# Optimization experiments

Hardware: AMD Instinct MI355X
Metric: run time of the kernel (lower is better)

Reference implementation:

```python
import jax, jax.numpy as jnp
import numpy as np

BOARD_H, BOARD_W = 10, 9
NUM_NODES = BOARD_H * BOARD_W  # 90
NUM_HEADS = 4


def _build_base_adjacency():
    adj = np.zeros((NUM_NODES, NUM_NODES), dtype=np.float32)
    for y in range(BOARD_H):
        for x in range(BOARD_W):
            idx = y * BOARD_W + x
            for dy, dx in [(0, 1), (0, -1), (1, 0), (-1, 0)]:
                ny, nx = y + dy, x + dx
                if 0 <= ny < BOARD_H and 0 <= nx < BOARD_W:
                    adj[idx, ny * BOARD_W + nx] = 1.0
            for nx in range(BOARD_W):
                if nx != x and abs(nx - x) <= 4:
                    nidx = y * BOARD_W + nx
                    adj[idx, nidx] = max(adj[idx, nidx], 1.0 / abs(nx - x))
            for ny in range(BOARD_H):
                if ny != y and abs(ny - y) <= 5:
                    nidx = ny * BOARD_W + x
                    adj[idx, nidx] = max(adj[idx, nidx], 1.0 / abs(ny - y))
            adj[idx, idx] = 1.0
    deg = np.clip(adj.sum(-1, keepdims=True), 1.0, None)
    return adj / deg  # (90, 90)


def _pos_encoding():
    px = (np.arange(BOARD_W, dtype=np.float32) / BOARD_W)
    py = (np.arange(BOARD_H, dtype=np.float32) / BOARD_H)
    gx = np.broadcast_to(px[None, :], (BOARD_H, BOARD_W)).reshape(-1)
    gy = np.broadcast_to(py[:, None], (BOARD_H, BOARD_W)).reshape(-1)
    return np.stack([gx, gy], axis=-1)  # (90, 2)


def _gat_layer(x, adj, W, a_src, a_dst, gamma, beta):
    B, N, _ = x.shape
    h = (x @ W).reshape(B, N, NUM_HEADS, -1)          # (B,N,H,D)
    s_src = jnp.einsum('bnhd,hd->bhn', h, a_src)       # (B,H,N)
    s_dst = jnp.einsum('bnhd,hd->bhn', h, a_dst)
    attn = s_src[..., :, None] + s_dst[..., None, :]   # (B,H,N,N)
    attn = jax.nn.leaky_relu(attn, 0.2)
    attn = jnp.where((adj == 0)[None, None], -jnp.inf, attn)
    attn = jax.nn.softmax(attn, axis=-1)
    attn = jnp.nan_to_num(attn, nan=0.0)
    out = jnp.einsum('bhij,bjhd->bihd', attn, h).reshape(B * N, -1)
    # BatchNorm1d in training mode: biased batch stats over (B*N)
    mean = out.mean(0)
    var = out.var(0)
    out = (out - mean) * jax.lax.rsqrt(var + 1e-5) * gamma + beta
    return jax.nn.relu(out.reshape(B, N, -1))


def setup_inputs() -> dict:
    key = jax.random.key(0)
    ks = jax.random.split(key, 16)
    B, F_in, Hd, Dout = 2048, 16, 64, 128
    hdim = Hd // NUM_HEADS
    p = lambda k, s: (jax.random.normal(k, s, dtype=jnp.float32) * 0.1)
    return {
        'board_planes': jax.random.uniform(ks[0], (B, 14, BOARD_H, BOARD_W), dtype=jnp.float32),
        'in_W': p(ks[1], (F_in, Hd)), 'in_b': p(ks[2], (Hd,)),
        'W0': p(ks[3], (Hd, Hd)), 'asrc0': p(ks[4], (NUM_HEADS, hdim)), 'adst0': p(ks[5], (NUM_HEADS, hdim)),
        'g0': jnp.ones((Hd,), jnp.float32), 'b0': jnp.zeros((Hd,), jnp.float32),
        'W1': p(ks[6], (Hd, Hd)), 'asrc1': p(ks[7], (NUM_HEADS, hdim)), 'adst1': p(ks[8], (NUM_HEADS, hdim)),
        'g1': jnp.ones((Hd,), jnp.float32), 'b1': jnp.zeros((Hd,), jnp.float32),
        'out_W': p(ks[9], (Hd, Dout)), 'out_b': p(ks[10], (Dout,)),
    }


def reference(board_planes, in_W, in_b, W0, asrc0, adst0, g0, b0,
              W1, asrc1, adst1, g1, b1, out_W, out_b):
    B = board_planes.shape[0]
    adj = jnp.asarray(_build_base_adjacency())            # (90,90), same for all batches
    nodes = board_planes.reshape(B, 14, NUM_NODES).transpose(0, 2, 1)  # (B,90,14)
    pos = jnp.broadcast_to(jnp.asarray(_pos_encoding())[None], (B, NUM_NODES, 2))
    x = jnp.concatenate([nodes, pos], axis=-1)            # (B,90,16)
    x = x @ in_W + in_b
    x = _gat_layer(x, adj, W0, asrc0, adst0, g0, b0)
    x = _gat_layer(x, adj, W1, asrc1, adst1, g1, b1)
    return x.mean(axis=1) @ out_W + out_b                 # (B,128)
```

## Files before the change

### kernel.cpp

```cpp
#include <hip/hip_runtime.h>
#include <cstdint>


#define BB   2048
#define NN   90
#define NP   96
#define CC   64
#define NH   4
#define HD   16
#define TPB  512
#define DOUT 128
#define SWP  72
#define SHP  72
#define PPITCH 24
#define NSLOT 19

typedef _Float16 f16;
typedef _Float16 f16x4 __attribute__((ext_vector_type(4)));
typedef _Float16 f16x8 __attribute__((ext_vector_type(8)));
typedef float f32x4 __attribute__((ext_vector_type(4)));
union U16x8 { f16x8 v; f16 e[8]; };
union U16x4 { f16x4 v; f16 e[4]; };

#define UNI_BYTES 19712
#define BIG_BYTES 27648

template <int LAYER>
__global__ __launch_bounds__(TPB, 6) void k_gat(
    const float* __restrict__ bp,
    const float* __restrict__ inW,
    const float* __restrict__ inb,
    const float* __restrict__ prevPre,
    const float* __restrict__ stPrev,
    const float* __restrict__ Wl,
    const float* __restrict__ asrc,
    const float* __restrict__ adst,
    float* __restrict__ outPre,
    float* __restrict__ partial,
    float* __restrict__ partialSq)
{
    __shared__ __align__(16) unsigned char uni[UNI_BYTES];
    __shared__ __align__(16) unsigned char big[BIG_BYTES];
    __shared__ float sAs[NH * HD], sAd[NH * HD];
    __shared__ float sSrc[NH][NN], sDst[NH][NN];
    __shared__ float sST[2 * CC];

    f16*   sWt  = (f16*)uni;
    float* sInW = (float*)(uni + 9216);
    float* sInb = (float*)(uni + 13312);
    float* sXr  = (float*)(uni + 13568);
    f16*   sPh  = (f16*)uni;
    float* sRa  = (float*)uni;
    float* sRb  = (float*)(uni + 8192);
    f16*   sx   = (f16*)big;
    float* shF  = (float*)big;

    const int b = blockIdx.x, t = threadIdx.x;
    const int cq = t & 15, ng = t >> 4;
    const int c4 = cq << 2;
    const int jcnt = (ng < NN - 64) ? 3 : 2;

    for (int i = t; i < CC * CC; i += TPB) {
        int k = i >> 6, c = i & 63;
        sWt[c * SWP + k] = (f16)Wl[i];
    }
    if (t < NH * HD) { sAs[t] = asrc[t]; sAd[t] = adst[t]; }

    if (t < (NP - NN) * (SHP / 4)) {
        int r = t / (SHP / 4), q = t % (SHP / 4);
        f16x4 z = {(f16)0, (f16)0, (f16)0, (f16)0};
        *(f16x4*)&sx[(NN + r) * SHP + q * 4] = z;
    }

    if (LAYER == 0) {
        for (int i = t; i < 16 * CC; i += TPB) sInW[i] = inW[i];
        if (t < CC) sInb[t] = inb[t];
        const float* bpb = bp + (size_t)b * (14 * NN);
        for (int i = t; i < 14 * NN; i += TPB) {
            int p = i / NN, n = i - p * NN;
            sXr[n * 17 + p] = bpb[i];
        }
        if (t < NN) {
            int y = t / 9, x = t - y * 9;
            sXr[t * 17 + 14] = (float)x / 9.0f;
            sXr[t * 17 + 15] = (float)y / 10.0f;
        }
    } else {
        if (t < 2 * CC) sST[t] = stPrev[t];
    }
    __syncthreads();

    if (LAYER == 0) {
        const int n0 = ng, n1 = ng + 32, n2 = (jcnt == 3) ? ng + 64 : ng;
        float acc[3][4] = {};
        #pragma unroll
        for (int k = 0; k < 16; k++) {
            float4 w = *(const float4*)&sInW[k * CC + c4];
            float x0 = sXr[n0 * 17 + k], x1 = sXr[n1 * 17 + k], x2 = sXr[n2 * 17 + k];
            acc[0][0] = fmaf(x0, w.x, acc[0][0]); acc[0][1] = fmaf(x0, w.y, acc[0][1]);
            acc[0][2] = fmaf(x0, w.z, acc[0][2]); acc[0][3] = fmaf(x0, w.w, acc[0][3]);
            acc[1][0] = fmaf(x1, w.x, acc[1][0]); acc[1][1] = fmaf(x1, w.y, acc[1][1]);
            acc[1][2] = fmaf(x1, w.z, acc[1][2]); acc[1][3] = fmaf(x1, w.w, acc[1][3]);
            acc[2][0] = fmaf(x2, w.x, acc[2][0]); acc[2][1] = fmaf(x2, w.y, acc[2][1]);
            acc[2][2] = fmaf(x2, w.z, acc[2][2]); acc[2][3] = fmaf(x2, w.w, acc[2][3]);
        }
        for (int j = 0; j < jcnt; j++) {
            int n = ng + 32 * j;
            f16x4 o;
            o.x = (f16)(acc[j][0] + sInb[c4 + 0]);
            o.y = (f16)(acc[j][1] + sInb[c4 + 1]);
            o.z = (f16)(acc[j][2] + sInb[c4 + 2]);
            o.w = (f16)(acc[j][3] + sInb[c4 + 3]);
            *(f16x4*)&sx[n * SHP + c4] = o;
        }
    } else {
        const float4* pv4 = (const float4*)(prevPre + (size_t)b * (NN * CC));
        for (int i4 = t; i4 < NN * CC / 4; i4 += TPB) {
            float4 v = pv4[i4];
            int n = i4 >> 4, c = (i4 & 15) << 2;
            float a0 = fmaf(v.x, sST[c + 0], sST[CC + c + 0]);
            float a1 = fmaf(v.y, sST[c + 1], sST[CC + c + 1]);
            float a2 = fmaf(v.z, sST[c + 2], sST[CC + c + 2]);
            float a3 = fmaf(v.w, sST[c + 3], sST[CC + c + 3]);
            f16x4 o;
            o.x = (f16)(a0 > 0.0f ? a0 : 0.0f);
            o.y = (f16)(a1 > 0.0f ? a1 : 0.0f);
            o.z = (f16)(a2 > 0.0f ? a2 : 0.0f);
            o.w = (f16)(a3 > 0.0f ? a3 : 0.0f);
            *(f16x4*)&sx[n * SHP + c] = o;
        }
    }
    __syncthreads();

    {
        const int w = t >> 6, lane = t & 63;
        const int lr = lane & 15, lg = lane >> 4;
        const int nt = w & 3, m0 = w >> 2;
        const f16x8 bf0 = *(const f16x8*)&sWt[(nt * 16 + lr) * SWP + lg * 8];
        const f16x8 bf1 = *(const f16x8*)&sWt[(nt * 16 + lr) * SWP + 32 + lg * 8];
        f16x8 af0[3], af1[3];
        #pragma unroll
        for (int mi = 0; mi < 3; mi++) {
            const int mt = m0 + 2 * mi;
            af0[mi] = *(const f16x8*)&sx[(mt * 16 + lr) * SHP + lg * 8];
            af1[mi] = *(const f16x8*)&sx[(mt * 16 + lr) * SHP + 32 + lg * 8];
        }
        __syncthreads();
        #pragma unroll
        for (int mi = 0; mi < 3; mi++) {
            const int mt = m0 + 2 * mi;
            f32x4 acc = {0.0f, 0.0f, 0.0f, 0.0f};
            acc = __builtin_amdgcn_mfma_f32_16x16x32_f16(af0[mi], bf0, acc, 0, 0, 0);
            acc = __builtin_amdgcn_mfma_f32_16x16x32_f16(af1[mi], bf1, acc, 0, 0, 0);
            const int row = mt * 16 + lg * 4, col = nt * 16 + lr;
            shF[(row + 0) * SHP + col] = acc[0];
            shF[(row + 1) * SHP + col] = acc[1];
            shF[(row + 2) * SHP + col] = acc[2];
            shF[(row + 3) * SHP + col] = acc[3];
        }
    }
    __syncthreads();

    if (t < NH * NN) {
        int hh = t / NN, n = t - hh * NN;
        const float4* hv = (const float4*)&shF[n * SHP + hh * HD];
        float a = 0.0f, d = 0.0f;
        #pragma unroll
        for (int m = 0; m < 4; m++) {
            float4 h4 = hv[m];
            a = fmaf(h4.x, sAs[hh * HD + 4 * m + 0], a);
            a = fmaf(h4.y, sAs[hh * HD + 4 * m + 1], a);
            a = fmaf(h4.z, sAs[hh * HD + 4 * m + 2], a);
            a = fmaf(h4.w, sAs[hh * HD + 4 * m + 3], a);
            d = fmaf(h4.x, sAd[hh * HD + 4 * m + 0], d);
            d = fmaf(h4.y, sAd[hh * HD + 4 * m + 1], d);
            d = fmaf(h4.z, sAd[hh * HD + 4 * m + 2], d);
            d = fmaf(h4.w, sAd[hh * HD + 4 * m + 3], d);
        }
        sSrc[hh][n] = a; sDst[hh][n] = d;
    }
    __syncthreads();

    if (t < NH * NN) {
        int hh = t / NN, n = t - hh * NN;
        int y = n / 9, x = n - y * 9;
        float si = sSrc[hh][n];
        float e[NSLOT];
        #pragma unroll
        for (int xx = 0; xx < 9; xx++) {
            int dx = xx > x ? xx - x : x - xx;
            float ee = si + sDst[hh][y * 9 + xx];
            ee = ee > 0.0f ? ee : 0.2f * ee;
            e[xx] = (dx <= 4) ? ee : -1e30f;
        }
        #pragma unroll
        for (int yy = 0; yy < 10; yy++) {
            int dy = yy > y ? yy - y : y - yy;
            float ee = si + sDst[hh][yy * 9 + x];
            ee = ee > 0.0f ? ee : 0.2f * ee;
            e[9 + yy] = (dy >= 1 && dy <= 5) ? ee : -1e30f;
        }
        float m = e[0];
        #pragma unroll
        for (int k = 1; k < NSLOT; k++) m = fmaxf(m, e[k]);
        float s = 0.0f;
        f16* pr = &sPh[(hh * NN + n) * PPITCH];
        #pragma unroll
        for (int k = 0; k < NSLOT; k++) {
            float p = __expf(e[k] - m);
            s += p;
            pr[k] = (f16)p;
        }
        sSrc[hh][n] = 1.0f / s;
    }
    __syncthreads();

    const int hh2 = cq >> 2;
    float lsum[4] = {}, lsq[4] = {};
    float* op = outPre + (size_t)b * (NN * CC);
    for (int j = 0; j < jcnt; j++) {
        int n = ng + 32 * j;
        int y = n / 9, x = n - y * 9;
        float inv = sSrc[hh2][n];
        const f16* pr = &sPh[(hh2 * NN + n) * PPITCH];
        U16x8 pA, pB; U16x4 pT;
        pA.v = *(const f16x8*)pr;
        pB.v = *(const f16x8*)(pr + 8);
        pT.v = *(const f16x4*)(pr + 16);
        float a0 = 0.0f, a1 = 0.0f, a2 = 0.0f, a3 = 0.0f;
        #pragma unroll
        for (int xx = 0; xx < 9; xx++) {
            float p = (xx < 8) ? (float)pA.e[xx] : (float)pB.e[0];
            float4 h4 = *(const float4*)&shF[(y * 9 + xx) * SHP + c4];
            a0 = fmaf(p, h4.x, a0); a1 = fmaf(p, h4.y, a1);
            a2 = fmaf(p, h4.z, a2); a3 = fmaf(p, h4.w, a3);
        }
        #pragma unroll
        for (int yy = 0; yy < 10; yy++) {
            int k = 9 + yy;
            float p = (k < 16) ? (float)pB.e[k - 8] : (float)pT.e[k - 16];
            float4 h4 = *(const float4*)&shF[(yy * 9 + x) * SHP + c4];
            a0 = fmaf(p, h4.x, a0); a1 = fmaf(p, h4.y, a1);
            a2 = fmaf(p, h4.z, a2); a3 = fmaf(p, h4.w, a3);
        }
        a0 *= inv; a1 *= inv; a2 *= inv; a3 *= inv;
        float4 o; o.x = a0; o.y = a1; o.z = a2; o.w = a3;
        *(float4*)&op[n * CC + c4] = o;
        lsum[0] += a0; lsum[1] += a1; lsum[2] += a2; lsum[3] += a3;
        lsq[0] = fmaf(a0, a0, lsq[0]); lsq[1] = fmaf(a1, a1, lsq[1]);
        lsq[2] = fmaf(a2, a2, lsq[2]); lsq[3] = fmaf(a3, a3, lsq[3]);
    }
    __syncthreads();

    #pragma unroll
    for (int q = 0; q < 4; q++) {
        sRa[ng * CC + c4 + q] = lsum[q];
        sRb[ng * CC + c4 + q] = lsq[q];
    }
    __syncthreads();
    if (t < CC) {
        float s = 0.0f, q2 = 0.0f;
        #pragma unroll
        for (int g = 0; g < 32; g++) {
            s  += sRa[g * CC + t];
            q2 += sRb[g * CC + t];
        }
        partial[(size_t)b * CC + t] = s;
        partialSq[(size_t)b * CC + t] = q2;
    }
}

__global__ __launch_bounds__(256) void k_stats(
    const float* __restrict__ partial, const float* __restrict__ partialSq,
    const float* __restrict__ gamma, const float* __restrict__ beta,
    float* __restrict__ st)
{
    const int c = blockIdx.x, t = threadIdx.x;
    float s = 0.0f, q = 0.0f;
    for (int b = t; b < BB; b += 256) {
        s += partial[(size_t)b * CC + c];
        q += partialSq[(size_t)b * CC + c];
    }
    __shared__ float rs[256], rq[256];
    rs[t] = s; rq[t] = q;
    __syncthreads();
    for (int o = 128; o > 0; o >>= 1) {
        if (t < o) { rs[t] += rs[t + o]; rq[t] += rq[t + o]; }
        __syncthreads();
    }
    if (t == 0) {
        const float cntInv = 1.0f / (float)(BB * NN);
        float mean = rs[0] * cntInv;
        float var  = rq[0] * cntInv - mean * mean;
        float sc = gamma[c] * rsqrtf(var + 1e-5f);
        st[c] = sc;
        st[CC + c] = beta[c] - mean * sc;
    }
}

__global__ __launch_bounds__(256) void k_final(
    const float* __restrict__ pre, const float* __restrict__ st,
    const float* __restrict__ outW, const float* __restrict__ outb,
    float* __restrict__ out)
{
    __shared__ float sM[CC];
    __shared__ float sPart[4][CC];
    const int b = blockIdx.x, t = threadIdx.x;
    const int c = t & 63, p = t >> 6;
    const float* pv = pre + (size_t)b * (NN * CC);
    float s = st[c], sft = st[CC + c];
    float a = 0.0f;
    int nBeg = p * 23, nEnd = nBeg + 23 < NN ? nBeg + 23 : NN;
    for (int n = nBeg; n < nEnd; n++) {
        float v = fmaf(pv[n * CC + c], s, sft);
        a += (v > 0.0f ? v : 0.0f);
    }
    sPart[p][c] = a;
    __syncthreads();
    if (t < CC)
        sM[t] = (sPart[0][t] + sPart[1][t] + sPart[2][t] + sPart[3][t]) * (1.0f / (float)NN);
    __syncthreads();
    if (t < DOUT) {
        float acc = outb[t];
        #pragma unroll
        for (int cc2 = 0; cc2 < CC; cc2++) acc = fmaf(sM[cc2], outW[cc2 * DOUT + t], acc);
        out[(size_t)b * DOUT + t] = acc;
    }
}

extern "C" void kernel_launch(void* const* d_in, const int* in_sizes, int n_in,
                              void* d_out, int out_size, void* d_ws, size_t ws_size,
                              hipStream_t stream) {
    (void)in_sizes; (void)n_in; (void)out_size; (void)ws_size;

    const float* bp   = (const float*)d_in[0];
    const float* inW  = (const float*)d_in[1];
    const float* inb  = (const float*)d_in[2];
    const float* W0   = (const float*)d_in[3];
    const float* as0  = (const float*)d_in[4];
    const float* ad0  = (const float*)d_in[5];
    const float* g0   = (const float*)d_in[6];
    const float* b0   = (const float*)d_in[7];
    const float* W1   = (const float*)d_in[8];
    const float* as1  = (const float*)d_in[9];
    const float* ad1  = (const float*)d_in[10];
    const float* g1   = (const float*)d_in[11];
    const float* b1   = (const float*)d_in[12];
    const float* outW = (const float*)d_in[13];
    const float* outb = (const float*)d_in[14];
    float* out = (float*)d_out;

    float* ws = (float*)d_ws;
    float* outPre    = ws;
    float* partial   = outPre + (size_t)BB * NN * CC;
    float* partialSq = partial + (size_t)BB * CC;
    float* st0       = partialSq + (size_t)BB * CC;
    float* st1       = st0 + 2 * CC;

    k_gat<0><<<BB, TPB, 0, stream>>>(bp, inW, inb, nullptr, nullptr,
                                     W0, as0, ad0, outPre, partial, partialSq);
    k_stats<<<CC, 256, 0, stream>>>(partial, partialSq, g0, b0, st0);
    k_gat<1><<<BB, TPB, 0, stream>>>(nullptr, nullptr, nullptr, outPre, st0,
                                     W1, as1, ad1, outPre, partial, partialSq);
    k_stats<<<CC, 256, 0, stream>>>(partial, partialSq, g1, b1, st1);
    k_final<<<BB, 256, 0, stream>>>(outPre, st1, outW, outb, out);
}
```

Before: 109.0 us.

## Shrink LDS footprint to raise occupancy and read weights from global

Merges the shared buffers into one smaller LDS region by narrowing pitches, storing the raw inputs and attention scores in fp16, and no longer staging the weight matrix, input weights, bias and attention vectors in LDS. Those are now read directly from global memory or cache. The launch bound rises from 6 to 8 blocks per CU. Softmax normalisation moves into the probability write, and the stats reduction uses wave shuffles before an 8-way LDS combine. The extra global reads of the weights and the fp16 score precision are the trade-offs, and a dead f16x4 loop is left behind.

```diff
diff --git a/kernel.cpp b/kernel.cpp
--- a/kernel.cpp
+++ b/kernel.cpp
@@ -10,23 +10,21 @@
 #define HD   16
 #define TPB  512
 #define DOUT 128
-#define SWP  72
-#define SHP  72
-#define PPITCH 24
+#define SXP  72
+#define SHP  68
+#define PPITCH 20
 #define NSLOT 19
 
 typedef _Float16 f16;
 typedef _Float16 f16x4 __attribute__((ext_vector_type(4)));
 typedef _Float16 f16x8 __attribute__((ext_vector_type(8)));
 typedef float f32x4 __attribute__((ext_vector_type(4)));
-union U16x8 { f16x8 v; f16 e[8]; };
 union U16x4 { f16x4 v; f16 e[4]; };
 
-#define UNI_BYTES 19712
-#define BIG_BYTES 27648
+#define LDS_BYTES 40832
 
 template <int LAYER>
-__global__ __launch_bounds__(TPB, 6) void k_gat(
+__global__ __launch_bounds__(TPB, 8) void k_gat(
     const float* __restrict__ bp,
     const float* __restrict__ inW,
     const float* __restrict__ inb,
@@ -39,51 +37,40 @@
     float* __restrict__ partial,
     float* __restrict__ partialSq)
 {
-    __shared__ __align__(16) unsigned char uni[UNI_BYTES];
-    __shared__ __align__(16) unsigned char big[BIG_BYTES];
-    __shared__ float sAs[NH * HD], sAd[NH * HD];
-    __shared__ float sSrc[NH][NN], sDst[NH][NN];
-    __shared__ float sST[2 * CC];
-
-    f16*   sWt  = (f16*)uni;
-    float* sInW = (float*)(uni + 9216);
-    float* sInb = (float*)(uni + 13312);
-    float* sXr  = (float*)(uni + 13568);
+    __shared__ __align__(16) unsigned char lds[LDS_BYTES];
+    float* shF  = (float*)lds;
+    f16*   sx   = (f16*)lds;
+    unsigned char* uni = lds + 24480;
+    f16*   sXr  = (f16*)uni;
     f16*   sPh  = (f16*)uni;
     float* sRa  = (float*)uni;
-    float* sRb  = (float*)(uni + 8192);
-    f16*   sx   = (f16*)big;
-    float* shF  = (float*)big;
+    float* sRb  = (float*)(uni + 2048);
+    f16*   sSrcH = (f16*)(lds + 38880);
+    f16*   sDstH = (f16*)(lds + 39600);
+    float* sST   = (float*)(lds + 40320);
 
     const int b = blockIdx.x, t = threadIdx.x;
     const int cq = t & 15, ng = t >> 4;
     const int c4 = cq << 2;
     const int jcnt = (ng < NN - 64) ? 3 : 2;
-
-    for (int i = t; i < CC * CC; i += TPB) {
-        int k = i >> 6, c = i & 63;
-        sWt[c * SWP + k] = (f16)Wl[i];
-    }
-    if (t < NH * HD) { sAs[t] = asrc[t]; sAd[t] = adst[t]; }
-
-    if (t < (NP - NN) * (SHP / 4)) {
-        int r = t / (SHP / 4), q = t % (SHP / 4);
+    const int lane = t & 63, wv = t >> 6;
+    const int lr = lane & 15, lg = lane >> 4;
+
+    if (t < (NP - NN) * (SXP / 4)) {
+        int r = t / (SXP / 4), q = t - r * (SXP / 4);
         f16x4 z = {(f16)0, (f16)0, (f16)0, (f16)0};
-        *(f16x4*)&sx[(NN + r) * SHP + q * 4] = z;
-    }
-
+        *(f16x4*)&sx[(NN + r) * SXP + q * 4] = z;
+    }
     if (LAYER == 0) {
-        for (int i = t; i < 16 * CC; i += TPB) sInW[i] = inW[i];
-        if (t < CC) sInb[t] = inb[t];
         const float* bpb = bp + (size_t)b * (14 * NN);
         for (int i = t; i < 14 * NN; i += TPB) {
             int p = i / NN, n = i - p * NN;
-            sXr[n * 17 + p] = bpb[i];
+            sXr[n * 17 + p] = (f16)bpb[i];
         }
         if (t < NN) {
             int y = t / 9, x = t - y * 9;
-            sXr[t * 17 + 14] = (float)x / 9.0f;
-            sXr[t * 17 + 15] = (float)y / 10.0f;
+            sXr[t * 17 + 14] = (f16)((float)x / 9.0f);
+            sXr[t * 17 + 15] = (f16)((float)y / 10.0f);
         }
     } else {
         if (t < 2 * CC) sST[t] = stPrev[t];
@@ -92,11 +79,14 @@
 
     if (LAYER == 0) {
         const int n0 = ng, n1 = ng + 32, n2 = (jcnt == 3) ? ng + 64 : ng;
+        const float4* inW4 = (const float4*)inW;
         float acc[3][4] = {};
-        #pragma unroll
+        #pragma unroll 4
         for (int k = 0; k < 16; k++) {
-            float4 w = *(const float4*)&sInW[k * CC + c4];
-            float x0 = sXr[n0 * 17 + k], x1 = sXr[n1 * 17 + k], x2 = sXr[n2 * 17 + k];
+            float4 w = inW4[k * 16 + cq];
+            float x0 = (float)sXr[n0 * 17 + k];
+            float x1 = (float)sXr[n1 * 17 + k];
+            float x2 = (float)sXr[n2 * 17 + k];
             acc[0][0] = fmaf(x0, w.x, acc[0][0]); acc[0][1] = fmaf(x0, w.y, acc[0][1]);
             acc[0][2] = fmaf(x0, w.z, acc[0][2]); acc[0][3] = fmaf(x0, w.w, acc[0][3]);
             acc[1][0] = fmaf(x1, w.x, acc[1][0]); acc[1][1] = fmaf(x1, w.y, acc[1][1]);
@@ -104,14 +94,15 @@
             acc[2][0] = fmaf(x2, w.x, acc[2][0]); acc[2][1] = fmaf(x2, w.y, acc[2][1]);
             acc[2][2] = fmaf(x2, w.z, acc[2][2]); acc[2][3] = fmaf(x2, w.w, acc[2][3]);
         }
+        float4 bias = *(const float4*)&inb[c4];
         for (int j = 0; j < jcnt; j++) {
             int n = ng + 32 * j;
             f16x4 o;
-            o.x = (f16)(acc[j][0] + sInb[c4 + 0]);
-            o.y = (f16)(acc[j][1] + sInb[c4 + 1]);
-            o.z = (f16)(acc[j][2] + sInb[c4 + 2]);
-            o.w = (f16)(acc[j][3] + sInb[c4 + 3]);
-            *(f16x4*)&sx[n * SHP + c4] = o;
+            o.x = (f16)(acc[j][0] + bias.x);
+            o.y = (f16)(acc[j][1] + bias.y);
+            o.z = (f16)(acc[j][2] + bias.z);
+            o.w = (f16)(acc[j][3] + bias.w);
+            *(f16x4*)&sx[n * SXP + c4] = o;
         }
     } else {
         const float4* pv4 = (const float4*)(prevPre + (size_t)b * (NN * CC));
@@ -127,23 +118,25 @@
             o.y = (f16)(a1 > 0.0f ? a1 : 0.0f);
             o.z = (f16)(a2 > 0.0f ? a2 : 0.0f);
             o.w = (f16)(a3 > 0.0f ? a3 : 0.0f);
-            *(f16x4*)&sx[n * SHP + c] = o;
+            *(f16x4*)&sx[n * SXP + c] = o;
         }
     }
     __syncthreads();
 
     {
-        const int w = t >> 6, lane = t & 63;
-        const int lr = lane & 15, lg = lane >> 4;
-        const int nt = w & 3, m0 = w >> 2;
-        const f16x8 bf0 = *(const f16x8*)&sWt[(nt * 16 + lr) * SWP + lg * 8];
-        const f16x8 bf1 = *(const f16x8*)&sWt[(nt * 16 + lr) * SWP + 32 + lg * 8];
+        const int nt = wv & 3, m0 = wv >> 2;
+        f16x8 bf0, bf1;
+        #pragma unroll
+        for (int j = 0; j < 8; j++) {
+            bf0[j] = (f16)Wl[(lg * 8 + j) * CC + nt * 16 + lr];
+            bf1[j] = (f16)Wl[(lg * 8 + j + 32) * CC + nt * 16 + lr];
+        }
         f16x8 af0[3], af1[3];
         #pragma unroll
         for (int mi = 0; mi < 3; mi++) {
             const int mt = m0 + 2 * mi;
-            af0[mi] = *(const f16x8*)&sx[(mt * 16 + lr) * SHP + lg * 8];
-            af1[mi] = *(const f16x8*)&sx[(mt * 16 + lr) * SHP + 32 + lg * 8];
+            af0[mi] = *(const f16x8*)&sx[(mt * 16 + lr) * SXP + lg * 8];
+            af1[mi] = *(const f16x8*)&sx[(mt * 16 + lr) * SXP + 32 + lg * 8];
         }
         __syncthreads();
         #pragma unroll
@@ -153,10 +146,9 @@
             acc = __builtin_amdgcn_mfma_f32_16x16x32_f16(af0[mi], bf0, acc, 0, 0, 0);
             acc = __builtin_amdgcn_mfma_f32_16x16x32_f16(af1[mi], bf1, acc, 0, 0, 0);
             const int row = mt * 16 + lg * 4, col = nt * 16 + lr;
-            shF[(row + 0) * SHP + col] = acc[0];
-            shF[(row + 1) * SHP + col] = acc[1];
-            shF[(row + 2) * SHP + col] = acc[2];
-            shF[(row + 3) * SHP + col] = acc[3];
+            #pragma unroll
+            for (int r = 0; r < 4; r++)
+                if (row + r < NN) shF[(row + r) * SHP + col] = acc[r];
         }
     }
     __syncthreads();
@@ -164,54 +156,67 @@
     if (t < NH * NN) {
         int hh = t / NN, n = t - hh * NN;
         const float4* hv = (const float4*)&shF[n * SHP + hh * HD];
+        const float4* av = (const float4*)(asrc + hh * HD);
+        const float4* dv = (const float4*)(adst + hh * HD);
         float a = 0.0f, d = 0.0f;
         #pragma unroll
         for (int m = 0; m < 4; m++) {
-            float4 h4 = hv[m];
-            a = fmaf(h4.x, sAs[hh * HD + 4 * m + 0], a);
-            a = fmaf(h4.y, sAs[hh * HD + 4 * m + 1], a);
-            a = fmaf(h4.z, sAs[hh * HD + 4 * m + 2], a);
-            a = fmaf(h4.w, sAs[hh * HD + 4 * m + 3], a);
-            d = fmaf(h4.x, sAd[hh * HD + 4 * m + 0], d);
-            d = fmaf(h4.y, sAd[hh * HD + 4 * m + 1], d);
-            d = fmaf(h4.z, sAd[hh * HD + 4 * m + 2], d);
-            d = fmaf(h4.w, sAd[hh * HD + 4 * m + 3], d);
-        }
-        sSrc[hh][n] = a; sDst[hh][n] = d;
+            float4 h4 = hv[m], am = av[m], dm = dv[m];
+            a = fmaf(h4.x, am.x, a); a = fmaf(h4.y, am.y, a);
+            a = fmaf(h4.z, am.z, a); a = fmaf(h4.w, am.w, a);
+            d = fmaf(h4.x, dm.x, d); d = fmaf(h4.y, dm.y, d);
+            d = fmaf(h4.z, dm.z, d); d = fmaf(h4.w, dm.w, d);
+        }
+        sSrcH[t] = (f16)a; sDstH[t] = (f16)d;
     }
     __syncthreads();
 
     if (t < NH * NN) {
         int hh = t / NN, n = t - hh * NN;
         int y = n / 9, x = n - y * 9;
-        float si = sSrc[hh][n];
+        float si = (float)sSrcH[t];
         float e[NSLOT];
         #pragma unroll
         for (int xx = 0; xx < 9; xx++) {
             int dx = xx > x ? xx - x : x - xx;
-            float ee = si + sDst[hh][y * 9 + xx];
+            float ee = si + (float)sDstH[hh * NN + y * 9 + xx];
             ee = ee > 0.0f ? ee : 0.2f * ee;
             e[xx] = (dx <= 4) ? ee : -1e30f;
         }
         #pragma unroll
         for (int yy = 0; yy < 10; yy++) {
             int dy = yy > y ? yy - y : y - yy;
-            float ee = si + sDst[hh][yy * 9 + x];
+            float ee = si + (float)sDstH[hh * NN + yy * 9 + x];
             ee = ee > 0.0f ? ee : 0.2f * ee;
             e[9 + yy] = (dy >= 1 && dy <= 5) ? ee : -1e30f;
         }
         float m = e[0];
         #pragma unroll
         for (int k = 1; k < NSLOT; k++) m = fmaxf(m, e[k]);
+        float p[NSLOT];
         float s = 0.0f;
-        f16* pr = &sPh[(hh * NN + n) * PPITCH];
-        #pragma unroll
-        for (int k = 0; k < NSLOT; k++) {
-            float p = __expf(e[k] - m);
-            s += p;
-            pr[k] = (f16)p;
-        }
-        sSrc[hh][n] = 1.0f / s;
+        #pragma unroll
+        for (int k = 0; k < NSLOT; k++) { p[k] = __expf(e[k] - m); s += p[k]; }
+        float inv = 1.0f / s;
+        f16* pr = &sPh[t * PPITCH];
+        #pragma unroll
+        for (int q = 0; q < 5; q++) {
+            f16x4 o;
+            o.x = (f16)(p[4 * q + 0] * inv);
+            o.y = (f16)(p[4 * q + 1] * inv);
+            o.z = (f16)(p[4 * q + 2] * inv);
+            o.w = (4 * q + 3 < NSLOT) ? (f16)(p[4 * q + 3] * inv) : (f16)0;
+        }
+        #pragma unroll
+        for (int q = 0; q < 5; q++) {
+            U16x4 o;
+            #pragma unroll
+            for (int j = 0; j < 4; j++) {
+                int k = 4 * q + j;
+                o.e[j] = (k < NSLOT) ? (f16)(p[k] * inv) : (f16)0;
+            }
+            *(f16x4*)&pr[4 * q] = o.v;
+        }
     }
     __syncthreads();
 
@@ -221,16 +226,18 @@
     for (int j = 0; j < jcnt; j++) {
         int n = ng + 32 * j;
         int y = n / 9, x = n - y * 9;
-        float inv = sSrc[hh2][n];
         const f16* pr = &sPh[(hh2 * NN + n) * PPITCH];
-        U16x8 pA, pB; U16x4 pT;
-        pA.v = *(const f16x8*)pr;
-        pB.v = *(const f16x8*)(pr + 8);
-        pT.v = *(const f16x4*)(pr + 16);
+        U16x4 P0, P1, P2, P3, P4;
+        P0.v = *(const f16x4*)&pr[0];
+        P1.v = *(const f16x4*)&pr[4];
+        P2.v = *(const f16x4*)&pr[8];
+        P3.v = *(const f16x4*)&pr[12];
+        P4.v = *(const f16x4*)&pr[16];
         float a0 = 0.0f, a1 = 0.0f, a2 = 0.0f, a3 = 0.0f;
         #pragma unroll
         for (int xx = 0; xx < 9; xx++) {
-            float p = (xx < 8) ? (float)pA.e[xx] : (float)pB.e[0];
+            float p = (xx < 4) ? (float)P0.e[xx]
+                    : (xx < 8) ? (float)P1.e[xx - 4] : (float)P2.e[0];
             float4 h4 = *(const float4*)&shF[(y * 9 + xx) * SHP + c4];
             a0 = fmaf(p, h4.x, a0); a1 = fmaf(p, h4.y, a1);
             a2 = fmaf(p, h4.z, a2); a3 = fmaf(p, h4.w, a3);
@@ -238,12 +245,12 @@
         #pragma unroll
         for (int yy = 0; yy < 10; yy++) {
             int k = 9 + yy;
-            float p = (k < 16) ? (float)pB.e[k - 8] : (float)pT.e[k - 16];
+            float p = (k < 12) ? (float)P2.e[k - 8]
+                    : (k < 16) ? (float)P3.e[k - 12] : (float)P4.e[k - 16];
             float4 h4 = *(const float4*)&shF[(yy * 9 + x) * SHP + c4];
             a0 = fmaf(p, h4.x, a0); a1 = fmaf(p, h4.y, a1);
             a2 = fmaf(p, h4.z, a2); a3 = fmaf(p, h4.w, a3);
         }
-        a0 *= inv; a1 *= inv; a2 *= inv; a3 *= inv;
         float4 o; o.x = a0; o.y = a1; o.z = a2; o.w = a3;
         *(float4*)&op[n * CC + c4] = o;
         lsum[0] += a0; lsum[1] += a1; lsum[2] += a2; lsum[3] += a3;
@@ -254,14 +261,24 @@
 
     #pragma unroll
     for (int q = 0; q < 4; q++) {
-        sRa[ng * CC + c4 + q] = lsum[q];
-        sRb[ng * CC + c4 + q] = lsq[q];
+        float v = lsum[q];
+        v += __shfl_xor(v, 16); v += __shfl_xor(v, 32);
+        lsum[q] = v;
+        float w2 = lsq[q];
+        w2 += __shfl_xor(w2, 16); w2 += __shfl_xor(w2, 32);
+        lsq[q] = w2;
+    }
+    if (lg == 0) {
+        float4 a; a.x = lsum[0]; a.y = lsum[1]; a.z = lsum[2]; a.w = lsum[3];
+        float4 c; c.x = lsq[0]; c.y = lsq[1]; c.z = lsq[2]; c.w = lsq[3];
+        *(float4*)&sRa[wv * CC + c4] = a;
+        *(float4*)&sRb[wv * CC + c4] = c;
     }
     __syncthreads();
     if (t < CC) {
         float s = 0.0f, q2 = 0.0f;
         #pragma unroll
-        for (int g = 0; g < 32; g++) {
+        for (int g = 0; g < 8; g++) {
             s  += sRa[g * CC + t];
             q2 += sRb[g * CC + t];
         }
```

Result: slower. 118.0 us (+8.3%).
